# Kernel tuning notes

Hardware: AMD Instinct MI355X
Metric: run time of the kernel (lower is better)

Reference implementation:

```python
import jax, jax.numpy as jnp
import numpy as np

EPS = 1e-8

def _ternary_linear(x, w):
    # Ternary quantization of weights: sign(w) where |w| > 0.5 * mean(|w|), else 0.
    alpha = jnp.mean(jnp.abs(w))
    w_t = jnp.sign(w) * (jnp.abs(w) > 0.5 * alpha).astype(w.dtype)
    # STE: forward uses ternary weights, backward passes grad straight to w.
    w_q = w + jax.lax.stop_gradient(w_t - w)
    # Custom RMS norm: ||x||_2 / sqrt(d), no learned scale.
    d = x.shape[-1]
    rms = jnp.sqrt(jnp.sum(x * x, axis=-1, keepdims=True)) / jnp.sqrt(jnp.asarray(d, x.dtype))
    x_norm = x / (rms + EPS)
    # F.linear(x, w): x @ w.T  -> [..., out]
    return jnp.einsum('bsd,fd->bsf', x_norm, w_q)

def setup_inputs() -> dict:
    key = jax.random.key(0)
    k1, k2, k3 = jax.random.split(key, 3)
    d_model, d_ff = 1024, 4096
    B, S = 4, 4096
    x = jax.random.normal(k1, (B, S, d_model), dtype=jnp.float32)
    w_up = jax.random.normal(k2, (d_ff, d_model), dtype=jnp.float32) * 0.02
    w_down = jax.random.normal(k3, (d_model, d_ff), dtype=jnp.float32) * 0.02
    return {"x": x, "w_up": w_up, "w_down": w_down}

def reference(x, w_up, w_down):
    h = jax.nn.gelu(_ternary_linear(x, w_up), approximate=False)  # exact erf GELU as torch F.gelu default
    return _ternary_linear(h, w_down)
```

## Files before the change

kernel.cpp:

```cpp
#include <hip/hip_runtime.h>
#include <hip/hip_bf16.h>
#include <stdint.h>


#define M_ROWS   16384
#define D_MODEL  1024
#define D_FF     4096
#define NW       (D_FF * D_MODEL)

typedef __attribute__((ext_vector_type(4))) int   i32x4;
typedef __attribute__((ext_vector_type(4))) float f32x4;

__device__ __forceinline__ void gload_lds16(const void* g, void* l) {
    __builtin_amdgcn_global_load_lds(
        (const __attribute__((address_space(1))) void*)g,
        (__attribute__((address_space(3))) void*)l, 16, 0, 0);
}

#define BAR()     __builtin_amdgcn_s_barrier()
#define VMCNT(n)  asm volatile("s_waitcnt vmcnt(" #n ")" ::: "memory")

__device__ __forceinline__ float gelu_fast(float v) {
    float w = v * v;
    float z = v * __builtin_fmaf(w, 0.07135481627f, 1.5957691216f);
    float e = __expf(-z);
    return v / (1.0f + e);
}
__device__ __forceinline__ int q8(float v) {
    int q = __float2int_rn(v);
    return (q > 127) ? 127 : ((q < -127) ? -127 : q);
}

__global__ __launch_bounds__(256) void absmean_reduce(const float* __restrict__ w,
                                                      double* __restrict__ asum) {
    const int n4 = NW / 4;
    float s = 0.f;
    const float4* w4 = (const float4*)w;
    for (int i = blockIdx.x * blockDim.x + threadIdx.x; i < n4;
         i += gridDim.x * blockDim.x) {
        float4 v = w4[i];
        s += fabsf(v.x) + fabsf(v.y) + fabsf(v.z) + fabsf(v.w);
    }
    #pragma unroll
    for (int off = 32; off > 0; off >>= 1) s += __shfl_down(s, off);
    __shared__ float sm[4];
    int lane = threadIdx.x & 63, wid = threadIdx.x >> 6;
    if (lane == 0) sm[wid] = s;
    __syncthreads();
    if (threadIdx.x == 0) {
        float t = sm[0] + sm[1] + sm[2] + sm[3];
        atomicAdd(asum, (double)t);
    }
}

__global__ __launch_bounds__(256) void quant_w8(const float* __restrict__ w,
                                                const double* __restrict__ asum,
                                                char* __restrict__ wq) {
    float thr = (float)(0.5 * (*asum) * (1.0 / (double)NW));
    int i = blockIdx.x * blockDim.x + threadIdx.x;
    float4 v = ((const float4*)w)[i];
    int b0 = (fabsf(v.x) > thr) ? (v.x > 0.f ? 1 : -1) : 0;
    int b1 = (fabsf(v.y) > thr) ? (v.y > 0.f ? 1 : -1) : 0;
    int b2 = (fabsf(v.z) > thr) ? (v.z > 0.f ? 1 : -1) : 0;
    int b3 = (fabsf(v.w) > thr) ? (v.w > 0.f ? 1 : -1) : 0;
    ((int*)wq)[i] = (b0 & 0xff) | ((b1 & 0xff) << 8) |
                    ((b2 & 0xff) << 16) | ((b3 & 0xff) << 24);
}

__global__ __launch_bounds__(256) void rmsnorm_xq(const float* __restrict__ x,
                                                  char* __restrict__ xq) {
    const int row = blockIdx.x;
    const float4* xr = (const float4*)(x + (size_t)row * D_MODEL);
    float4 v = xr[threadIdx.x];
    float ss = v.x * v.x + v.y * v.y + v.z * v.z + v.w * v.w;
    #pragma unroll
    for (int off = 32; off > 0; off >>= 1) ss += __shfl_down(ss, off);
    __shared__ float sm[4];
    int lane = threadIdx.x & 63, wid = threadIdx.x >> 6;
    if (lane == 0) sm[wid] = ss;
    __syncthreads();
    float tot = sm[0] + sm[1] + sm[2] + sm[3];
    float s = 24.0f / (sqrtf(tot) * (1.0f / 32.0f) + 1e-8f);
    int b0 = q8(v.x * s), b1 = q8(v.y * s), b2 = q8(v.z * s), b3 = q8(v.w * s);
    ((int*)(xq + (size_t)row * D_MODEL))[threadIdx.x] =
        (b0 & 0xff) | ((b1 & 0xff) << 8) | ((b2 & 0xff) << 16) | ((b3 & 0xff) << 24);
}

__global__ __launch_bounds__(256) void rowscale_hq(const char* __restrict__ hq,
                                                   float* __restrict__ rs) {
    const int row = blockIdx.x;
    const int4* hr = (const int4*)(hq + (size_t)row * D_FF);
    int4 d = hr[threadIdx.x];
    float ss = 0.f;
    #pragma unroll
    for (int w = 0; w < 4; ++w) {
        int dw = (w == 0) ? d.x : (w == 1) ? d.y : (w == 2) ? d.z : d.w;
        #pragma unroll
        for (int b = 0; b < 4; ++b) {
            int q = (int)(char)((dw >> (8 * b)) & 0xff);
            ss += (float)(q * q);
        }
    }
    #pragma unroll
    for (int off = 32; off > 0; off >>= 1) ss += __shfl_down(ss, off);
    __shared__ float sm[4];
    int lane = threadIdx.x & 63, wid = threadIdx.x >> 6;
    if (lane == 0) sm[wid] = ss;
    __syncthreads();
    if (threadIdx.x == 0) {
        float tot = sm[0] + sm[1] + sm[2] + sm[3];
        rs[row] = 1.0f / (sqrtf(tot) * (1.0f / 64.0f) + 1e-8f);
    }
}

template <int EPI, int KDIM, int NBLKN>
__global__ __launch_bounds__(512) void gemm_i8t(const char* __restrict__ A,
                                                const char* __restrict__ B,
                                                char* __restrict__ Cq,
                                                float* __restrict__ Cf,
                                                const float* __restrict__ rowscale,
                                                int nwg) {
    constexpr int BUFB = 24576;
    constexpr int NT = KDIM / 64;
    __shared__ char smem[3 * BUFB];

    const int tid = threadIdx.x;
    const int bid = blockIdx.x;
    const int swz = (bid & 7) * (nwg >> 3) + (bid >> 3);
    const uint m0 = (uint)(swz / NBLKN) * 256u;
    const uint n0 = (uint)(swz % NBLKN) * 128u;

    const int lane = tid & 63;
    const int wid  = tid >> 6;
    const int wm   = wid >> 1;
    const int wn   = wid & 1;
    const int lr   = lane & 15;
    const int lk   = lane >> 4;

    uint aOff[2], bOff;
    #pragma unroll
    for (int inst = 0; inst < 2; ++inst) {
        uint s = (uint)tid + (uint)inst * 512u;
        uint row = s >> 2, ch = s & 3u;
        uint src = ((ch ^ ((row >> 1) & 3u)) << 4);
        aOff[inst] = (m0 + row) * (uint)KDIM + src;
    }
    {
        uint row = (uint)tid >> 2, ch = (uint)tid & 3u;
        uint src = ((ch ^ ((row >> 1) & 3u)) << 4);
        bOff = (n0 + row) * (uint)KDIM + src;
    }
    const uint dstOff = (uint)tid * 16u;

    uint offA[4], offB[4];
    #pragma unroll
    for (int i = 0; i < 4; ++i) {
        uint rowa = (uint)(wm * 64 + i * 16 + lr);
        offA[i] = rowa * 64u + (((uint)lk ^ ((rowa >> 1) & 3u)) << 4);
        uint rowb = (uint)(wn * 64 + i * 16 + lr);
        offB[i] = 16384u + rowb * 64u + (((uint)lk ^ ((rowb >> 1) & 3u)) << 4);
    }

    i32x4 acc[4][4];
    #pragma unroll
    for (int mi = 0; mi < 4; ++mi)
        #pragma unroll
        for (int ni = 0; ni < 4; ++ni)
            acc[mi][ni] = (i32x4){0, 0, 0, 0};

    #pragma unroll
    for (int tt = 0; tt < 2; ++tt) {
        char* sb = smem + tt * BUFB;
        const uint k0 = (uint)tt * 64u;
        gload_lds16(A + aOff[0] + k0, sb +     0 + dstOff);
        gload_lds16(A + aOff[1] + k0, sb +  8192 + dstOff);
        gload_lds16(B + bOff    + k0, sb + 16384 + dstOff);
    }
    VMCNT(3);
    BAR();

    int cur = 0, stg = 2;
    #pragma unroll 1
    for (int t = 0; t < NT; ++t) {
        const char* cb = smem + cur * BUFB;
        char* sb = smem + stg * BUFB;
        const uint kc = (uint)(t + 2) * 64u;
        const bool doS = (t + 2 < NT);
        i32x4 av[4], bv[4];

        #pragma unroll
        for (int i = 0; i < 4; ++i) av[i] = *(const i32x4*)(cb + offA[i]);
        #pragma unroll
        for (int i = 0; i < 4; ++i) bv[i] = *(const i32x4*)(cb + offB[i]);
        if (doS) {
            gload_lds16(A + aOff[0] + kc, sb +     0 + dstOff);
            gload_lds16(A + aOff[1] + kc, sb +  8192 + dstOff);
            gload_lds16(B + bOff    + kc, sb + 16384 + dstOff);
        }
        __builtin_amdgcn_s_setprio(1);
        #pragma unroll
        for (int mi = 0; mi < 4; ++mi)
            #pragma unroll
            for (int ni = 0; ni < 4; ++ni)
                acc[mi][ni] = __builtin_amdgcn_mfma_i32_16x16x64_i8(
                    av[mi], bv[ni], acc[mi][ni], 0, 0, 0);
        __builtin_amdgcn_s_setprio(0);

        if (doS) { VMCNT(3); } else { VMCNT(0); }
        BAR();
        cur = (cur == 2) ? 0 : cur + 1;
        stg = (stg == 2) ? 0 : stg + 1;
    }

    constexpr uint N = (uint)NBLKN * 128u;
    #pragma unroll
    for (int mi = 0; mi < 4; ++mi) {
        #pragma unroll
        for (int j = 0; j < 4; ++j) {
            const uint gr = m0 + (uint)(wm * 64 + mi * 16 + lk * 4 + j);
            float s = 0.f;
            if (EPI == 1) s = rowscale[gr];
            #pragma unroll
            for (int ni = 0; ni < 4; ++ni) {
                const uint gc = n0 + (uint)(wn * 64 + ni * 16 + lr);
                if (EPI == 0) {
                    float g = gelu_fast((float)acc[mi][ni][j] * (1.0f / 24.0f));
                    Cq[gr * N + gc] = (char)q8(g);
                } else {
                    Cf[gr * N + gc] = (float)acc[mi][ni][j] * s;
                }
            }
        }
    }
}

extern "C" void kernel_launch(void* const* d_in, const int* in_sizes, int n_in,
                              void* d_out, int out_size, void* d_ws, size_t ws_size,
                              hipStream_t stream) {
    const float* x    = (const float*)d_in[0];
    const float* w_up = (const float*)d_in[1];
    const float* w_dn = (const float*)d_in[2];
    float* out = (float*)d_out;

    uint8_t* ws = (uint8_t*)d_ws;
    char* hq  = (char*)(ws);
    char* xq  = (char*)(ws + 67108864);
    char* wqu = (char*)(ws + 67108864 + 16777216);
    char* wqd = (char*)(ws + 67108864 + 16777216 + 4194304);
    float*  rs   = (float*)(ws + 67108864 + 16777216 + 2 * 4194304);
    double* alph = (double*)(ws + 67108864 + 16777216 + 2 * 4194304 + 65536);

    hipMemsetAsync(alph, 0, 16, stream);

    absmean_reduce<<<256, 256, 0, stream>>>(w_up, alph + 0);
    absmean_reduce<<<256, 256, 0, stream>>>(w_dn, alph + 1);
    quant_w8<<<NW / 1024, 256, 0, stream>>>(w_up, alph + 0, wqu);
    quant_w8<<<NW / 1024, 256, 0, stream>>>(w_dn, alph + 1, wqd);
    rmsnorm_xq<<<M_ROWS, 256, 0, stream>>>(x, xq);

    gemm_i8t<0, D_MODEL, 32><<<2048, 512, 0, stream>>>(
        xq, wqu, hq, nullptr, nullptr, 2048);

    rowscale_hq<<<M_ROWS, 256, 0, stream>>>(hq, rs);

    gemm_i8t<1, D_FF, 8><<<512, 512, 0, stream>>>(
        hq, wqd, nullptr, out, rs, 512);
}
```

Before: 224.0 us.

## Use 256x256 tile double-buffered int8 GEMM for up-projection

Adds a dedicated up-projection GEMM kernel with 256x256 output tiles (8 warps as 2x4, 8x4 MFMA accumulators per warp) instead of 256x128. It uses two LDS buffers instead of three and splits each k-step into two MFMA halves, with the next tile's loads issued between them. The larger tile halves the number of workgroups and raises arithmetic intensity per LDS byte, at the cost of more accumulator registers (128 VGPRs for acc) and shallower prefetch. The down-projection kernel loses its EPI template parameter but is otherwise unchanged.

```diff
diff --git a/kernel.cpp b/kernel.cpp
--- a/kernel.cpp
+++ b/kernel.cpp
@@ -113,10 +113,130 @@
     }
 }
 
-template <int EPI, int KDIM, int NBLKN>
+template <int KDIM, int NBLKN>
+__global__ __launch_bounds__(512) void gemm_i8big(const char* __restrict__ A,
+                                                  const char* __restrict__ B,
+                                                  char* __restrict__ Cq,
+                                                  int nwg) {
+    constexpr int BUFB = 32768;
+    constexpr int NT = KDIM / 64;
+    __shared__ char smem[2 * BUFB];
+
+    const int tid = threadIdx.x;
+    const int bid = blockIdx.x;
+    const int swz = (bid & 7) * (nwg >> 3) + (bid >> 3);
+    const uint m0 = (uint)(swz / NBLKN) * 256u;
+    const uint n0 = (uint)(swz % NBLKN) * 256u;
+
+    const int lane = tid & 63;
+    const int wid  = tid >> 6;
+    const int wm   = wid >> 2;
+    const int wn   = wid & 3;
+    const int lr   = lane & 15;
+    const int lk   = lane >> 4;
+
+    uint aOff[2], bOff[2];
+    #pragma unroll
+    for (int inst = 0; inst < 2; ++inst) {
+        uint s = (uint)tid + (uint)inst * 512u;
+        uint row = s >> 2, ch = s & 3u;
+        uint src = ((ch ^ ((row >> 1) & 3u)) << 4);
+        aOff[inst] = (m0 + row) * (uint)KDIM + src;
+        bOff[inst] = (n0 + row) * (uint)KDIM + src;
+    }
+    const uint dstOff = (uint)tid * 16u;
+
+    uint offA[8], offB[4];
+    #pragma unroll
+    for (int i = 0; i < 8; ++i) {
+        uint row = (uint)(wm * 128 + i * 16 + lr);
+        offA[i] = row * 64u + (((uint)lk ^ ((row >> 1) & 3u)) << 4);
+    }
+    #pragma unroll
+    for (int i = 0; i < 4; ++i) {
+        uint row = (uint)(wn * 64 + i * 16 + lr);
+        offB[i] = 16384u + row * 64u + (((uint)lk ^ ((row >> 1) & 3u)) << 4);
+    }
+
+    i32x4 acc[8][4];
+    #pragma unroll
+    for (int mi = 0; mi < 8; ++mi)
+        #pragma unroll
+        for (int ni = 0; ni < 4; ++ni)
+            acc[mi][ni] = (i32x4){0, 0, 0, 0};
+
+    {
+        gload_lds16(A + aOff[0], smem +     0 + dstOff);
+        gload_lds16(A + aOff[1], smem +  8192 + dstOff);
+        gload_lds16(B + bOff[0], smem + 16384 + dstOff);
+        gload_lds16(B + bOff[1], smem + 24576 + dstOff);
+    }
+    VMCNT(0);
+    BAR();
+
+    #pragma unroll 1
+    for (int t = 0; t < NT; ++t) {
+        const char* cb = smem + (t & 1) * BUFB;
+        char* sb = smem + ((t + 1) & 1) * BUFB;
+        const uint kc = (uint)(t + 1) * 64u;
+        const bool doS = (t + 1 < NT);
+        i32x4 av[4], bv[4];
+
+        #pragma unroll
+        for (int i = 0; i < 4; ++i) av[i] = *(const i32x4*)(cb + offA[i]);
+        #pragma unroll
+        for (int i = 0; i < 4; ++i) bv[i] = *(const i32x4*)(cb + offB[i]);
+        if (doS) {
+            gload_lds16(A + aOff[0] + kc, sb +    0 + dstOff);
+            gload_lds16(A + aOff[1] + kc, sb + 8192 + dstOff);
+        }
+        __builtin_amdgcn_s_setprio(1);
+        #pragma unroll
+        for (int mi = 0; mi < 4; ++mi)
+            #pragma unroll
+            for (int ni = 0; ni < 4; ++ni)
+                acc[mi][ni] = __builtin_amdgcn_mfma_i32_16x16x64_i8(
+                    av[mi], bv[ni], acc[mi][ni], 0, 0, 0);
+        __builtin_amdgcn_s_setprio(0);
+
+        #pragma unroll
+        for (int i = 0; i < 4; ++i) av[i] = *(const i32x4*)(cb + offA[4 + i]);
+        if (doS) {
+            gload_lds16(B + bOff[0] + kc, sb + 16384 + dstOff);
+            gload_lds16(B + bOff[1] + kc, sb + 24576 + dstOff);
+        }
+        __builtin_amdgcn_s_setprio(1);
+        #pragma unroll
+        for (int mi = 0; mi < 4; ++mi)
+            #pragma unroll
+            for (int ni = 0; ni < 4; ++ni)
+                acc[4 + mi][ni] = __builtin_amdgcn_mfma_i32_16x16x64_i8(
+                    av[mi], bv[ni], acc[4 + mi][ni], 0, 0, 0);
+        __builtin_amdgcn_s_setprio(0);
+
+        if (doS) { VMCNT(0); }
+        BAR();
+    }
+
+    constexpr uint N = (uint)NBLKN * 256u;
+    #pragma unroll
+    for (int mi = 0; mi < 8; ++mi) {
+        #pragma unroll
+        for (int j = 0; j < 4; ++j) {
+            const uint gr = m0 + (uint)(wm * 128 + mi * 16 + lk * 4 + j);
+            #pragma unroll
+            for (int ni = 0; ni < 4; ++ni) {
+                const uint gc = n0 + (uint)(wn * 64 + ni * 16 + lr);
+                float g = gelu_fast((float)acc[mi][ni][j] * (1.0f / 24.0f));
+                Cq[gr * N + gc] = (char)q8(g);
+            }
+        }
+    }
+}
+
+template <int KDIM, int NBLKN>
 __global__ __launch_bounds__(512) void gemm_i8t(const char* __restrict__ A,
                                                 const char* __restrict__ B,
-                                                char* __restrict__ Cq,
                                                 float* __restrict__ Cf,
                                                 const float* __restrict__ rowscale,
                                                 int nwg) {
@@ -218,17 +338,11 @@
         #pragma unroll
         for (int j = 0; j < 4; ++j) {
             const uint gr = m0 + (uint)(wm * 64 + mi * 16 + lk * 4 + j);
-            float s = 0.f;
-            if (EPI == 1) s = rowscale[gr];
+            float s = rowscale[gr];
             #pragma unroll
             for (int ni = 0; ni < 4; ++ni) {
                 const uint gc = n0 + (uint)(wn * 64 + ni * 16 + lr);
-                if (EPI == 0) {
-                    float g = gelu_fast((float)acc[mi][ni][j] * (1.0f / 24.0f));
-                    Cq[gr * N + gc] = (char)q8(g);
-                } else {
-                    Cf[gr * N + gc] = (float)acc[mi][ni][j] * s;
-                }
+                Cf[gr * N + gc] = (float)acc[mi][ni][j] * s;
             }
         }
     }
@@ -258,11 +372,9 @@
     quant_w8<<<NW / 1024, 256, 0, stream>>>(w_dn, alph + 1, wqd);
     rmsnorm_xq<<<M_ROWS, 256, 0, stream>>>(x, xq);
 
-    gemm_i8t<0, D_MODEL, 32><<<2048, 512, 0, stream>>>(
-        xq, wqu, hq, nullptr, nullptr, 2048);
+    gemm_i8big<D_MODEL, 16><<<1024, 512, 0, stream>>>(xq, wqu, hq, 1024);
 
     rowscale_hq<<<M_ROWS, 256, 0, stream>>>(hq, rs);
 
-    gemm_i8t<1, D_FF, 8><<<512, 512, 0, stream>>>(
-        hq, wqd, nullptr, out, rs, 512);
-}
+    gemm_i8t<D_FF, 8><<<512, 512, 0, stream>>>(hq, wqd, out, rs, 512);
+}
```

After: 228.0 us. No clear change (+1.8%).
